# Performance work log

Measured on AMD Instinct MI355X. Metric: run time of the kernel, lower is better.

Reference implementation:

```python
import jax, jax.numpy as jnp
import numpy as np

MARGIN = 0.3  # hard-coded in all three MarginRankingLoss instances


def setup_inputs() -> dict:
    key = jax.random.key(0)
    k1, k2, k3, k4 = jax.random.split(key, 4)
    n, d, num_ids = 4096, 2048, 100
    inputs = jax.random.normal(k1, (n, d), dtype=jnp.float32)
    targets_a = jax.random.randint(k2, (n,), 0, num_ids, dtype=jnp.int64)
    targets_b = jax.random.randint(k3, (n,), 0, num_ids, dtype=jnp.int64)
    lam = jax.random.uniform(k4, (), dtype=jnp.float32)
    epoch = 60
    return {"inputs": inputs, "targets_a": targets_a, "targets_b": targets_b,
            "lam": lam, "epoch": epoch}


def reference(inputs, targets_a, targets_b, lam, epoch):
    # pairwise euclidean distance: dist[i,j] = ||x_i - x_j||
    sq = jnp.sum(inputs * inputs, axis=1)                      # [n]
    dist = sq[:, None] + sq[None, :] - 2.0 * (inputs @ inputs.T)
    dist = jnp.sqrt(jnp.clip(dist, 1e-12))                     # [n, n]

    ma = targets_a[:, None] == targets_a[None, :]
    mb = targets_b[:, None] == targets_b[None, :]
    m_same_ab = ma & mb                                        # same a AND b (incl. diagonal)
    m_same_or = (ma & ~mb) | (~ma & mb)                        # exactly one of a/b matches
    m_dif_ab = ~ma & ~mb                                       # neither matches

    ninf = -jnp.inf
    pinf = jnp.inf
    hp = jnp.max(jnp.where(m_same_ab, dist, ninf), axis=1)     # hardest positive
    hn = jnp.min(jnp.where(m_dif_ab, dist, pinf), axis=1)      # hardest negative
    max_or = jnp.max(jnp.where(m_same_or, dist, ninf), axis=1)
    min_or = jnp.min(jnp.where(m_same_or, dist, pinf), axis=1)

    use_or = m_same_or.any(axis=1) & (epoch > 50)
    sp = jnp.where(use_or, max_or, hp)
    sn = jnp.where(use_or, min_or, hn)

    # MarginRankingLoss(x1, x2, y=1) = mean(relu(x2 - x1 + margin))
    loss_1 = jnp.mean(jnp.maximum(0.0, hp - hn + MARGIN))
    loss_2 = jnp.mean(jnp.maximum(0.0, sp - hn + MARGIN))
    loss_3 = jnp.mean(jnp.maximum(0.0, hp - sn + MARGIN))
    return loss_1 + loss_2 + loss_3
```

## Files before the change

### kernel.cpp

```cpp
#include <hip/hip_runtime.h>
#include <hip/hip_bf16.h>

#define NROW 4096
#define KDIM 2048
#define ROWB (KDIM * 2)
#define BT 256
#define BK 32
#define NT (KDIM / BK)
#define KTBUF 32768
#define AB_OFF 16384
#define PHI(r) ((((r) >> 1) & 3) << 4)

typedef __attribute__((ext_vector_type(8))) short bf16x8;
typedef __attribute__((ext_vector_type(4))) float f32x4;
typedef __attribute__((ext_vector_type(4))) unsigned short u16x4;

#define MFMA16(a, b, c) __builtin_amdgcn_mfma_f32_16x16x32_bf16((a), (b), (c), 0, 0, 0)

__device__ __forceinline__ unsigned short f2bf(float x) {
    unsigned u = __float_as_uint(x);
    unsigned r = (u + 0x7FFFu + ((u >> 16) & 1u)) >> 16;
    return (unsigned short)r;
}
__device__ __forceinline__ float bf2f(unsigned short b) {
    return __uint_as_float(((unsigned)b) << 16);
}

__global__ __launch_bounds__(256) void k_convert(const float* __restrict__ X,
                                                 unsigned short* __restrict__ Xb,
                                                 float* __restrict__ sqv) {
    const int row = blockIdx.x;
    const int t = threadIdx.x;
    const float4* xr = (const float4*)(X + (size_t)row * KDIM);
    unsigned short* br = Xb + (size_t)row * KDIM;
    float acc = 0.f;
#pragma unroll
    for (int it = 0; it < 2; ++it) {
        int idx = t * 2 + it;
        float4 v = xr[idx];
        u16x4 b;
        b.x = f2bf(v.x); b.y = f2bf(v.y); b.z = f2bf(v.z); b.w = f2bf(v.w);
        float f0 = bf2f(b.x), f1 = bf2f(b.y), f2 = bf2f(b.z), f3 = bf2f(b.w);
        acc += f0 * f0 + f1 * f1 + f2 * f2 + f3 * f3;
        *(u16x4*)(br + idx * 4) = b;
    }
#pragma unroll
    for (int s = 32; s > 0; s >>= 1) acc += __shfl_xor(acc, s);
    __shared__ float red[4];
    const int lane = t & 63, wid = t >> 6;
    if (lane == 0) red[wid] = acc;
    __syncthreads();
    if (t == 0) sqv[row] = red[0] + red[1] + red[2] + red[3];
}

__global__ __launch_bounds__(256) void k_init(unsigned* hp, unsigned* hn,
                                              unsigned* mor, unsigned* mir,
                                              float* out) {
    int i = blockIdx.x * 256 + threadIdx.x;
    hp[i] = 0u;
    hn[i] = 0x7F800000u;
    mor[i] = 0u;
    mir[i] = 0x7F800000u;
    if (i == 0) out[0] = 0.f;
}

__global__ __launch_bounds__(512, 2) void k_gemm(const unsigned short* __restrict__ Xb,
                                                 const float* __restrict__ sqv,
                                                 const int* __restrict__ ta,
                                                 const int* __restrict__ tb,
                                                 unsigned int* __restrict__ hp,
                                                 unsigned int* __restrict__ hn,
                                                 unsigned int* __restrict__ mor,
                                                 unsigned int* __restrict__ mir) {
    __shared__ char lds[3 * KTBUF];
    const int bi = blockIdx.x >> 4;
    const int bj = blockIdx.x & 15;
    const int t = threadIdx.x;
    const int lane = t & 63;
    const int w = t >> 6;
    const int wm = w >> 2;
    const int wn = w & 3;
    const int l15 = lane & 15;
    const int kg16 = (lane >> 4) * 16;
    const char* xbase = (const char*)Xb;

    const int swz = ((l15 >> 1) & 3) << 4;
    const int akbase = (wm * 128 + l15) * 64 + (kg16 ^ swz);
    const int bkbase = AB_OFF + (wn * 64 + l15) * 64 + (kg16 ^ swz);

    f32x4 acc[8][4] = {};

#define STAGE(tt, sb3)                                                        \
    do {                                                                      \
        _Pragma("unroll")                                                     \
        for (int isb_ = 0; isb_ < 2; ++isb_) {                                \
            _Pragma("unroll")                                                 \
            for (int q_ = 0; q_ < 2; ++q_) {                                  \
                const int row_ = q_ * 128 + (t >> 2);                         \
                const int gr_ = (isb_ ? bj : bi) * BT + row_;                 \
                const char* gsrc_ = xbase + (size_t)gr_ * ROWB +              \
                                    (size_t)(tt) * 64 +                       \
                                    (((t & 3) * 16) ^ PHI(row_));             \
                char* ldst_ = lds + (sb3) * KTBUF + isb_ * AB_OFF +           \
                              row_ * 64 + (t & 3) * 16;                       \
                __builtin_amdgcn_global_load_lds(                             \
                    (const __attribute__((address_space(1))) void*)gsrc_,     \
                    (__attribute__((address_space(3))) void*)ldst_, 16, 0, 0);\
            }                                                                 \
        }                                                                     \
    } while (0)

    STAGE(0, 0);
    STAGE(1, 1);

    int r3 = 0, s3 = 2;
    for (int tk = 0; tk < NT; ++tk) {
        if (tk < NT - 1)
            asm volatile("s_waitcnt vmcnt(4)" ::: "memory");
        else
            asm volatile("s_waitcnt vmcnt(0)" ::: "memory");
        __builtin_amdgcn_s_barrier();

        const char* buf = lds + r3 * KTBUF;
        bf16x8 af[8], bfr[4];
#pragma unroll
        for (int m = 0; m < 8; ++m)
            af[m] = *(const bf16x8*)(buf + akbase + m * 1024);
#pragma unroll
        for (int n = 0; n < 4; ++n)
            bfr[n] = *(const bf16x8*)(buf + bkbase + n * 1024);

        if (tk + 2 < NT) STAGE(tk + 2, s3);

#pragma unroll
        for (int m = 0; m < 8; ++m)
#pragma unroll
            for (int n = 0; n < 4; ++n)
                acc[m][n] = MFMA16(af[m], bfr[n], acc[m][n]);

        r3 = (r3 == 2) ? 0 : r3 + 1;
        s3 = (s3 == 2) ? 0 : s3 + 1;
    }
#undef STAGE

    float sqj[4];
    int taj[4], tbj[4];
#pragma unroll
    for (int n = 0; n < 4; ++n) {
        int j = bj * BT + wn * 64 + n * 16 + l15;
        sqj[n] = sqv[j];
        taj[n] = ta[j];
        tbj[n] = tb[j];
    }
    const float INF = __uint_as_float(0x7F800000u);
#pragma unroll
    for (int m = 0; m < 8; ++m) {
#pragma unroll
        for (int reg = 0; reg < 4; ++reg) {
            const int i = bi * BT + wm * 128 + m * 16 + (lane >> 4) * 4 + reg;
            const float sqi = sqv[i];
            const int tai = ta[i], tbi = tb[i];
            float vhp = 0.f, vhn = INF, vmo = 0.f, vmi = INF;
#pragma unroll
            for (int n = 0; n < 4; ++n) {
                float d2 = fmaxf(sqi + sqj[n] - 2.f * acc[m][n][reg], 1e-12f);
                bool ma = (tai == taj[n]), mb = (tbi == tbj[n]);
                if (ma && mb) {
                    vhp = fmaxf(vhp, d2);
                } else if (ma != mb) {
                    vmo = fmaxf(vmo, d2);
                    vmi = fminf(vmi, d2);
                } else {
                    vhn = fminf(vhn, d2);
                }
            }
#pragma unroll
            for (int s = 1; s < 16; s <<= 1) {
                vhp = fmaxf(vhp, __shfl_xor(vhp, s, 16));
                vhn = fminf(vhn, __shfl_xor(vhn, s, 16));
                vmo = fmaxf(vmo, __shfl_xor(vmo, s, 16));
                vmi = fminf(vmi, __shfl_xor(vmi, s, 16));
            }
            if (l15 == 0) {
                if (vhp > 0.f) atomicMax(&hp[i], __float_as_uint(vhp));
                if (vhn < INF) atomicMin(&hn[i], __float_as_uint(vhn));
                if (vmo > 0.f) {
                    atomicMax(&mor[i], __float_as_uint(vmo));
                    atomicMin(&mir[i], __float_as_uint(vmi));
                }
            }
        }
    }
}

__global__ __launch_bounds__(256) void k_final(const unsigned* __restrict__ hp,
                                               const unsigned* __restrict__ hn,
                                               const unsigned* __restrict__ mor,
                                               const unsigned* __restrict__ mir,
                                               const int* __restrict__ epoch_p,
                                               float* __restrict__ out) {
    const int t = threadIdx.x;
    const int i = blockIdx.x * 256 + t;
    const bool eok = (*epoch_p > 50);
    const unsigned morb = mor[i];
    float fhp = sqrtf(__uint_as_float(hp[i]));
    float fhn = sqrtf(__uint_as_float(hn[i]));
    bool use_or = (morb != 0u) && eok;
    float sp = use_or ? sqrtf(__uint_as_float(morb)) : fhp;
    float sn = use_or ? sqrtf(__uint_as_float(mir[i])) : fhn;
    float s = fmaxf(0.f, fhp - fhn + 0.3f) + fmaxf(0.f, sp - fhn + 0.3f) +
              fmaxf(0.f, fhp - sn + 0.3f);
#pragma unroll
    for (int sh = 32; sh > 0; sh >>= 1) s += __shfl_xor(s, sh);
    __shared__ float red[4];
    const int lane = t & 63, wid = t >> 6;
    if (lane == 0) red[wid] = s;
    __syncthreads();
    if (t == 0)
        atomicAdd(out, (red[0] + red[1] + red[2] + red[3]) * (1.f / 4096.f));
}

extern "C" void kernel_launch(void* const* d_in, const int* in_sizes, int n_in,
                              void* d_out, int out_size, void* d_ws, size_t ws_size,
                              hipStream_t stream) {
    const float* X = (const float*)d_in[0];
    const int* ta = (const int*)d_in[1];
    const int* tb = (const int*)d_in[2];
    const int* epoch_p = (const int*)d_in[4];
    float* out = (float*)d_out;

    char* ws = (char*)d_ws;
    unsigned short* Xb = (unsigned short*)ws;
    size_t off = (size_t)NROW * KDIM * sizeof(unsigned short);
    float* sqv = (float*)(ws + off); off += (size_t)NROW * 4;
    unsigned* hp = (unsigned*)(ws + off); off += (size_t)NROW * 4;
    unsigned* hn = (unsigned*)(ws + off); off += (size_t)NROW * 4;
    unsigned* mor = (unsigned*)(ws + off); off += (size_t)NROW * 4;
    unsigned* mir = (unsigned*)(ws + off); off += (size_t)NROW * 4;

    k_convert<<<NROW, 256, 0, stream>>>(X, Xb, sqv);
    k_init<<<NROW / 256, 256, 0, stream>>>(hp, hn, mor, mir, out);
    k_gemm<<<(NROW / BT) * (NROW / BT), 512, 0, stream>>>(Xb, sqv, ta, tb,
                                                          hp, hn, mor, mir);
    k_final<<<NROW / 256, 256, 0, stream>>>(hp, hn, mor, mir, epoch_p, out);
}
```

Baseline: 100.3 us.

## Exploit distance-matrix symmetry by computing only upper-triangular tiles with column reductions

Switches the Gram GEMM to compute only upper-triangular 128x128 tiles, since the pairwise distance matrix is symmetric. Each off-diagonal tile now also reduces along columns and updates the per-column hardest-positive, hardest-negative and one-match max/min through atomics. Tiles shrink from 256 to 128 with 256-thread blocks, which gives enough blocks for the triangular grid. The intent is to roughly halve the MFMA work and global loads, at the cost of smaller tiles with less data reuse, more atomics, and a serial loop to decode the triangular block index.

New measurement: 93.11 us. 1.08x faster.

```diff
diff --git a/kernel.cpp b/kernel.cpp
--- a/kernel.cpp
+++ b/kernel.cpp
@@ -4,11 +4,12 @@
 #define NROW 4096
 #define KDIM 2048
 #define ROWB (KDIM * 2)
-#define BT 256
+#define BT 128
+#define NB (NROW / BT)
 #define BK 32
 #define NT (KDIM / BK)
-#define KTBUF 32768
-#define AB_OFF 16384
+#define KTBUF 16384
+#define AB_OFF 8192
 #define PHI(r) ((((r) >> 1) & 3) << 4)
 
 typedef __attribute__((ext_vector_type(8))) short bf16x8;
@@ -64,7 +65,7 @@
     if (i == 0) out[0] = 0.f;
 }
 
-__global__ __launch_bounds__(512, 2) void k_gemm(const unsigned short* __restrict__ Xb,
+__global__ __launch_bounds__(256, 3) void k_gemm(const unsigned short* __restrict__ Xb,
                                                  const float* __restrict__ sqv,
                                                  const int* __restrict__ ta,
                                                  const int* __restrict__ tb,
@@ -73,22 +74,25 @@
                                                  unsigned int* __restrict__ mor,
                                                  unsigned int* __restrict__ mir) {
     __shared__ char lds[3 * KTBUF];
-    const int bi = blockIdx.x >> 4;
-    const int bj = blockIdx.x & 15;
+    int rem = blockIdx.x;
+    int bi = 0;
+    while (rem >= NB - bi) { rem -= NB - bi; ++bi; }
+    const int bj = bi + rem;
+
     const int t = threadIdx.x;
     const int lane = t & 63;
     const int w = t >> 6;
-    const int wm = w >> 2;
-    const int wn = w & 3;
+    const int wm = w >> 1;
+    const int wn = w & 1;
     const int l15 = lane & 15;
     const int kg16 = (lane >> 4) * 16;
     const char* xbase = (const char*)Xb;
 
     const int swz = ((l15 >> 1) & 3) << 4;
-    const int akbase = (wm * 128 + l15) * 64 + (kg16 ^ swz);
+    const int akbase = (wm * 64 + l15) * 64 + (kg16 ^ swz);
     const int bkbase = AB_OFF + (wn * 64 + l15) * 64 + (kg16 ^ swz);
 
-    f32x4 acc[8][4] = {};
+    f32x4 acc[4][4] = {};
 
 #define STAGE(tt, sb3)                                                        \
     do {                                                                      \
@@ -96,7 +100,7 @@
         for (int isb_ = 0; isb_ < 2; ++isb_) {                                \
             _Pragma("unroll")                                                 \
             for (int q_ = 0; q_ < 2; ++q_) {                                  \
-                const int row_ = q_ * 128 + (t >> 2);                         \
+                const int row_ = q_ * 64 + (t >> 2);                          \
                 const int gr_ = (isb_ ? bj : bi) * BT + row_;                 \
                 const char* gsrc_ = xbase + (size_t)gr_ * ROWB +              \
                                     (size_t)(tt) * 64 +                       \
@@ -122,9 +126,9 @@
         __builtin_amdgcn_s_barrier();
 
         const char* buf = lds + r3 * KTBUF;
-        bf16x8 af[8], bfr[4];
-#pragma unroll
-        for (int m = 0; m < 8; ++m)
+        bf16x8 af[4], bfr[4];
+#pragma unroll
+        for (int m = 0; m < 4; ++m)
             af[m] = *(const bf16x8*)(buf + akbase + m * 1024);
 #pragma unroll
         for (int n = 0; n < 4; ++n)
@@ -133,7 +137,7 @@
         if (tk + 2 < NT) STAGE(tk + 2, s3);
 
 #pragma unroll
-        for (int m = 0; m < 8; ++m)
+        for (int m = 0; m < 4; ++m)
 #pragma unroll
             for (int n = 0; n < 4; ++n)
                 acc[m][n] = MFMA16(af[m], bfr[n], acc[m][n]);
@@ -153,11 +157,18 @@
         tbj[n] = tb[j];
     }
     const float INF = __uint_as_float(0x7F800000u);
-#pragma unroll
-    for (int m = 0; m < 8; ++m) {
+
+    float chp[4], chn[4], cmo[4], cmi[4];
+#pragma unroll
+    for (int n = 0; n < 4; ++n) {
+        chp[n] = 0.f; chn[n] = INF; cmo[n] = 0.f; cmi[n] = INF;
+    }
+
+#pragma unroll
+    for (int m = 0; m < 4; ++m) {
 #pragma unroll
         for (int reg = 0; reg < 4; ++reg) {
-            const int i = bi * BT + wm * 128 + m * 16 + (lane >> 4) * 4 + reg;
+            const int i = bi * BT + wm * 64 + m * 16 + (lane >> 4) * 4 + reg;
             const float sqi = sqv[i];
             const int tai = ta[i], tbi = tb[i];
             float vhp = 0.f, vhn = INF, vmo = 0.f, vmi = INF;
@@ -167,11 +178,15 @@
                 bool ma = (tai == taj[n]), mb = (tbi == tbj[n]);
                 if (ma && mb) {
                     vhp = fmaxf(vhp, d2);
+                    chp[n] = fmaxf(chp[n], d2);
                 } else if (ma != mb) {
                     vmo = fmaxf(vmo, d2);
                     vmi = fminf(vmi, d2);
+                    cmo[n] = fmaxf(cmo[n], d2);
+                    cmi[n] = fminf(cmi[n], d2);
                 } else {
                     vhn = fminf(vhn, d2);
+                    chn[n] = fminf(chn[n], d2);
                 }
             }
 #pragma unroll
@@ -187,6 +202,26 @@
                 if (vmo > 0.f) {
                     atomicMax(&mor[i], __float_as_uint(vmo));
                     atomicMin(&mir[i], __float_as_uint(vmi));
+                }
+            }
+        }
+    }
+
+    if (bi != bj) {
+#pragma unroll
+        for (int n = 0; n < 4; ++n) {
+            float a = chp[n], b = chn[n], c = cmo[n], d = cmi[n];
+            a = fmaxf(a, __shfl_xor(a, 16)); a = fmaxf(a, __shfl_xor(a, 32));
+            b = fminf(b, __shfl_xor(b, 16)); b = fminf(b, __shfl_xor(b, 32));
+            c = fmaxf(c, __shfl_xor(c, 16)); c = fmaxf(c, __shfl_xor(c, 32));
+            d = fminf(d, __shfl_xor(d, 16)); d = fminf(d, __shfl_xor(d, 32));
+            if (lane < 16) {
+                const int j = bj * BT + wn * 64 + n * 16 + lane;
+                if (a > 0.f) atomicMax(&hp[j], __float_as_uint(a));
+                if (b < INF) atomicMin(&hn[j], __float_as_uint(b));
+                if (c > 0.f) {
+                    atomicMax(&mor[j], __float_as_uint(c));
+                    atomicMin(&mir[j], __float_as_uint(d));
                 }
             }
         }
@@ -240,7 +275,7 @@
 
     k_convert<<<NROW, 256, 0, stream>>>(X, Xb, sqv);
     k_init<<<NROW / 256, 256, 0, stream>>>(hp, hn, mor, mir, out);
-    k_gemm<<<(NROW / BT) * (NROW / BT), 512, 0, stream>>>(Xb, sqv, ta, tb,
-                                                          hp, hn, mor, mir);
+    k_gemm<<<(NB * (NB + 1)) / 2, 256, 0, stream>>>(Xb, sqv, ta, tb,
+                                                    hp, hn, mor, mir);
     k_final<<<NROW / 256, 256, 0, stream>>>(hp, hn, mor, mir, epoch_p, out);
 }
```
